# Performance work log

Hardware: AMD Instinct MI355X
Metric: run time of the kernel (lower is better)

## Reference

```python
import jax, jax.numpy as jnp
import numpy as np

B, S, D = 4, 2048, 1024
H, DH = 16, 64
THETA = 10000.0


def _rope_tables(seq_len, dim):
    # freqs_cis = exp(i * t * f), here as cos/sin tables, shape [S, dim//2]
    freqs = 1.0 / (THETA ** (jnp.arange(0, dim, 2, dtype=jnp.float32) / dim))
    ang = jnp.outer(jnp.arange(seq_len, dtype=jnp.float32), freqs)
    return jnp.cos(ang), jnp.sin(ang)


def _apply_rope(x, cos, sin):
    # x: [B,S,H,DH]; pairs are interleaved (x[...,2i], x[...,2i+1])
    xe = x[..., 0::2]
    xo = x[..., 1::2]
    c = cos[None, :, None, :]
    s = sin[None, :, None, :]
    out = jnp.stack([xe * c - xo * s, xe * s + xo * c], axis=-1)
    return out.reshape(x.shape).astype(x.dtype)


def setup_inputs() -> dict:
    key = jax.random.key(0)
    ks = jax.random.split(key, 5)
    x = jax.random.normal(ks[0], (B, S, D), dtype=jnp.float32)
    Wq = jax.random.normal(ks[1], (D, D), dtype=jnp.float32) * 0.02
    Wk = jax.random.normal(ks[2], (D, D), dtype=jnp.float32) * 0.02
    Wv = jax.random.normal(ks[3], (D, D), dtype=jnp.float32) * 0.02
    Wo = jax.random.normal(ks[4], (D, D), dtype=jnp.float32) * 0.02
    lambdas = jnp.zeros((2,), dtype=jnp.float32)
    return {"x": x, "Wq": Wq, "Wk": Wk, "Wv": Wv, "Wo": Wo, "lambdas": lambdas}


def reference(x, Wq, Wk, Wv, Wo, lambdas):
    scale = 1.0 / np.sqrt(DH)
    q = (x @ Wq.T).reshape(B, S, H, DH)
    k = (x @ Wk.T).reshape(B, S, H, DH)
    v = (x @ Wv.T).reshape(B, S, H, DH)
    cos, sin = _rope_tables(S, DH)
    q = _apply_rope(q, cos, sin)
    k = _apply_rope(k, cos, sin)
    # explicit QK^T with causal mask, softmax, then @V (dropout is identity in eval)
    attn = jnp.einsum('bshd,bthd->bhst', q, k) * scale  # [B,H,S,S]
    causal = jnp.tril(jnp.ones((S, S), dtype=bool))
    attn = jnp.where(causal[None, None], attn, -jnp.inf)
    probs = jax.nn.softmax(attn, axis=-1)
    head_out = jnp.einsum('bhst,bthd->bshd', probs, v)  # [B,S,H,DH]
    out = head_out.reshape(B, S, D) @ Wo.T
    return out
```

## Files before the change

kernel.cpp:

```cpp
#include <hip/hip_runtime.h>
#include <math.h>

static constexpr int Bsz = 4, Sq = 2048, Dm = 1024, NH = 16, DHd = 64;
static constexpr int Mrows = Bsz * Sq;
static constexpr float ROPE_LN = 0.14391156831212787f;
static constexpr float QSCALE = 0.18033688011112043f;

typedef _Float16 half8 __attribute__((ext_vector_type(8)));
typedef _Float16 half4v __attribute__((ext_vector_type(4)));
typedef __fp16 fp16x2 __attribute__((ext_vector_type(2)));
typedef float f32x4 __attribute__((ext_vector_type(4)));

__device__ __forceinline__ void gl_lds16(const void* g, void* l) {
    __builtin_amdgcn_global_load_lds(
        (const __attribute__((address_space(1))) void*)g,
        (__attribute__((address_space(3))) void*)l, 16, 0, 0);
}

__device__ __forceinline__ float exp2_hw(float x) {
    float r;
    asm volatile("v_exp_f32 %0, %1" : "=v"(r) : "v"(x));
    return r;
}

__global__ __launch_bounds__(256) void prep_kernel(
    const float* __restrict__ x,
    const float* __restrict__ Wq, const float* __restrict__ Wk,
    const float* __restrict__ Wv, const float* __restrict__ Wo,
    _Float16* __restrict__ xh,
    _Float16* __restrict__ Wqh, _Float16* __restrict__ Wkh,
    _Float16* __restrict__ Wvh, _Float16* __restrict__ Woh,
    float2* __restrict__ rope)
{
    const int i = blockIdx.x * 256 + threadIdx.x;
    if (i < 2097152) {
        const float4 v = ((const float4*)x)[i];
        half4v hv;
        hv[0] = (_Float16)v.x; hv[1] = (_Float16)v.y;
        hv[2] = (_Float16)v.z; hv[3] = (_Float16)v.w;
        ((half4v*)xh)[i] = hv;
    } else if (i < 3145728) {
        const int w = (i - 2097152) >> 18;
        const int off = (i - 2097152) & 262143;
        const float* s = (w == 0) ? Wq : (w == 1) ? Wk : (w == 2) ? Wv : Wo;
        _Float16* d = (w == 0) ? Wqh : (w == 1) ? Wkh : (w == 2) ? Wvh : Woh;
        const float sc = (w == 0) ? QSCALE : 1.0f;
        const float4 v = ((const float4*)s)[off];
        half4v hv;
        hv[0] = (_Float16)(v.x * sc); hv[1] = (_Float16)(v.y * sc);
        hv[2] = (_Float16)(v.z * sc); hv[3] = (_Float16)(v.w * sc);
        ((half4v*)d)[off] = hv;
    } else {
        const int t = i - 3145728;
        const int pos = t >> 5, j = t & 31;
        const float f = expf(-ROPE_LN * (float)(2 * j));
        const float a = (float)pos * f;
        rope[t] = make_float2(cosf(a), sinf(a));
    }
}

template <typename OutT, int MODE>
__device__ __forceinline__ void mfma_gemm_body(
    _Float16 (*As)[128 * 32], _Float16 (*Bs)[128 * 32],
    const _Float16* __restrict__ A, const _Float16* __restrict__ W,
    OutT* __restrict__ C, const float2* __restrict__ rope, int K, int N,
    int m0, int n0)
{
    const int tid = threadIdx.x;
    const int wave = tid >> 6, lane = tid & 63;
    const int quad = lane >> 4, l16 = lane & 15;
    const int wm = (wave >> 2) * 64;
    const int wn = (wave & 3) * 32;

    const int rr = tid >> 2, cp = tid & 3;
    const int cc = cp ^ ((rr >> 1) & 3);
    const _Float16* gA = A + (size_t)(m0 + rr) * K + cc * 8;
    const _Float16* gB = W + (size_t)(n0 + rr) * K + cc * 8;
    const int lOff = wave * 512;

    const int sw = (l16 >> 1) & 3;
    int offA[4], offB[2];
    #pragma unroll
    for (int t = 0; t < 4; ++t)
        offA[t] = (wm + t * 16 + l16) * 32 + ((quad ^ sw) * 8);
    #pragma unroll
    for (int t = 0; t < 2; ++t)
        offB[t] = (wn + t * 16 + l16) * 32 + ((quad ^ sw) * 8);

    f32x4 acc[4][2];
    #pragma unroll
    for (int im = 0; im < 4; ++im)
        #pragma unroll
        for (int nb = 0; nb < 2; ++nb)
            #pragma unroll
            for (int r = 0; r < 4; ++r) acc[im][nb][r] = 0.f;

    for (int k0 = 0; k0 < K; k0 += 64) {
        __syncthreads();
        #pragma unroll
        for (int kh = 0; kh < 2; ++kh) {
            gl_lds16(gA + k0 + kh * 32, &As[kh][lOff]);
            gl_lds16(gB + k0 + kh * 32, &Bs[kh][lOff]);
        }
        __syncthreads();

        #pragma unroll
        for (int kh = 0; kh < 2; ++kh) {
            half8 a[4], b[2];
            #pragma unroll
            for (int t = 0; t < 4; ++t)
                a[t] = *(const half8*)&As[kh][offA[t]];
            #pragma unroll
            for (int t = 0; t < 2; ++t)
                b[t] = *(const half8*)&Bs[kh][offB[t]];
            #pragma unroll
            for (int im = 0; im < 4; ++im)
                #pragma unroll
                for (int nb = 0; nb < 2; ++nb)
                    acc[im][nb] = __builtin_amdgcn_mfma_f32_16x16x32_f16(
                        a[im], b[nb], acc[im][nb], 0, 0, 0);
        }
    }

    #pragma unroll
    for (int nb = 0; nb < 2; ++nb) {
        const int n = n0 + wn + nb * 16 + l16;
        if constexpr (MODE == 2) {
            const int hb = ((m0 + wm) >> 11) * 16 + (n >> 6);
            const int dh = n & 63;
            const int tb = (m0 + wm) & (Sq - 1);
            half8 v0, v1;
            #pragma unroll
            for (int r = 0; r < 4; ++r)
                #pragma unroll
                for (int im = 0; im < 4; ++im) {
                    const int idx = r * 4 + im;
                    const _Float16 h = (_Float16)acc[im][nb][r];
                    if (idx < 8) v0[idx] = h; else v1[idx - 8] = h;
                }
            _Float16* dst = C + (((size_t)hb * 64 + dh) << 11) + tb + quad * 16;
            *(half8*)dst = v0;
            *(half8*)(dst + 8) = v1;
        } else {
            const int j = (n & 63) >> 1;
            #pragma unroll
            for (int im = 0; im < 4; ++im) {
                #pragma unroll
                for (int r = 0; r < 4; ++r) {
                    const int m = m0 + wm + im * 16 + quad * 4 + r;
                    float v = acc[im][nb][r];
                    if constexpr (MODE == 1) {
                        const int pos = m & (Sq - 1);
                        const float2 cs = rope[pos * 32 + j];
                        const float vp = __shfl_xor(v, 1);
                        v = (n & 1) ? (vp * cs.y + v * cs.x)
                                    : (v * cs.x - vp * cs.y);
                        C[(size_t)m * N + n] = (_Float16)v;
                    } else {
                        C[(size_t)m * N + n] = v;
                    }
                }
            }
        }
    }
}

__device__ __forceinline__ void xcd_swizzle(int& m0, int& n0) {
    const int orig = blockIdx.x + (blockIdx.y << 3);
    const int xcd = orig & 7, j = orig >> 3;
    m0 = (xcd * 8 + (j >> 3)) * 128;
    n0 = (j & 7) * 128;
}

__global__ __launch_bounds__(512) void qkv_mfma_kernel(
    const _Float16* __restrict__ xh,
    const _Float16* __restrict__ Wq, const _Float16* __restrict__ Wk,
    const _Float16* __restrict__ Wv,
    _Float16* __restrict__ Qo, _Float16* __restrict__ Ko,
    _Float16* __restrict__ VTp, const float2* __restrict__ rope)
{
    __shared__ _Float16 As[2][128 * 32];
    __shared__ _Float16 Bs[2][128 * 32];
    int m0, n0;
    xcd_swizzle(m0, n0);
    const int z = blockIdx.z;
    if (z == 0)
        mfma_gemm_body<_Float16, 1>(As, Bs, xh, Wq, Qo, rope, Dm, Dm, m0, n0);
    else if (z == 1)
        mfma_gemm_body<_Float16, 1>(As, Bs, xh, Wk, Ko, rope, Dm, Dm, m0, n0);
    else
        mfma_gemm_body<_Float16, 2>(As, Bs, xh, Wv, VTp, nullptr, Dm, Dm,
                                    m0, n0);
}

__global__ __launch_bounds__(512) void oproj_mfma_kernel(
    const _Float16* __restrict__ HOh, const _Float16* __restrict__ Wo,
    float* __restrict__ out)
{
    __shared__ _Float16 As[2][128 * 32];
    __shared__ _Float16 Bs[2][128 * 32];
    int m0, n0;
    xcd_swizzle(m0, n0);
    mfma_gemm_body<float, 0>(As, Bs, HOh, Wo, out, nullptr, Dm, Dm, m0, n0);
}

__global__ __launch_bounds__(256) void attn_mfma_kernel(
    const _Float16* __restrict__ Q, const _Float16* __restrict__ K,
    const _Float16* __restrict__ VT, _Float16* __restrict__ HO)
{
    __shared__ _Float16 Ks[2][64 * 64];
    __shared__ _Float16 Vs[2][64 * 64];
    __shared__ _Float16 Ps[4][32][72];

    const int tid = threadIdx.x;
    const int wave = tid >> 6, lane = tid & 63;
    const int quad = lane >> 4, l16 = lane & 15;
    const int id = blockIdx.x;
    const int hb = id & 63;
    const int qi = 15 - (id >> 6);
    const int h = hb & 15, b = hb >> 4;
    const int q0 = qi * 128;
    const size_t base = (size_t)b * Sq * Dm + (size_t)h * DHd;
    const size_t vtbase = (size_t)hb * 64 * Sq;

    half8 ones;
    #pragma unroll
    for (int i = 0; i < 8; ++i) ones[i] = (_Float16)1.0f;

    half8 aQ[2][2];
    #pragma unroll
    for (int mf = 0; mf < 2; ++mf) {
        const _Float16* qrow =
            Q + base + (size_t)(q0 + wave * 32 + mf * 16 + l16) * Dm + quad * 8;
        aQ[mf][0] = *(const half8*)(qrow);
        aQ[mf][1] = *(const half8*)(qrow + 32);
    }

    f32x4 Oacc[2][4];
    #pragma unroll
    for (int mf = 0; mf < 2; ++mf)
        #pragma unroll
        for (int nb = 0; nb < 4; ++nb)
            #pragma unroll
            for (int r = 0; r < 4; ++r) Oacc[mf][nb][r] = 0.f;
    f32x4 lacc[2];
    #pragma unroll
    for (int mf = 0; mf < 2; ++mf)
        #pragma unroll
        for (int r = 0; r < 4; ++r) lacc[mf][r] = 0.f;

    auto stage_tile = [&](int t0, int buf) {
        #pragma unroll
        for (int i = 0; i < 2; ++i) {
            const int F = (wave * 2 + i) * 64 + lane;
            const int r = F >> 3;
            const int cl = (F & 7) ^ (r & 7);
            gl_lds16(K + base + (size_t)(t0 + r) * Dm + cl * 8,
                     &Ks[buf][(wave * 2 + i) * 512]);
            gl_lds16(VT + vtbase + ((size_t)r << 11) + t0 + cl * 8,
                     &Vs[buf][(wave * 2 + i) * 512]);
        }
    };

    auto do_tile = [&](int buf, int dd, bool diag) {
        const _Float16* Kb = Ks[buf];
        const _Float16* Vb = Vs[buf];

        f32x4 sacc[2][4];
        #pragma unroll
        for (int mf = 0; mf < 2; ++mf)
            #pragma unroll
            for (int nb = 0; nb < 4; ++nb)
                #pragma unroll
                for (int r = 0; r < 4; ++r) sacc[mf][nb][r] = 0.f;
        __builtin_amdgcn_s_setprio(1);
        #pragma unroll
        for (int kstep = 0; kstep < 2; ++kstep) {
            #pragma unroll
            for (int nb = 0; nb < 4; ++nb) {
                const int krow = nb * 16 + l16;
                const int kch = (kstep * 4 + quad) ^ (krow & 7);
                const half8 bK = *(const half8*)&Kb[krow * 64 + kch * 8];
                #pragma unroll
                for (int mf = 0; mf < 2; ++mf)
                    sacc[mf][nb] = __builtin_amdgcn_mfma_f32_16x16x32_f16(
                        aQ[mf][kstep], bK, sacc[mf][nb], 0, 0, 0);
            }
        }
        __builtin_amdgcn_s_setprio(0);

        #pragma unroll
        for (int mf = 0; mf < 2; ++mf)
            #pragma unroll
            for (int r = 0; r < 4; ++r) {
                float e[4];
                #pragma unroll
                for (int nb = 0; nb < 4; ++nb) {
                    float v = sacc[mf][nb][r];
                    if (diag && (nb * 16 + l16 + dd >
                                 wave * 32 + mf * 16 + quad * 4 + r))
                        v = -1.0e4f;
                    e[nb] = exp2_hw(v);
                }
                const fp16x2 lo = __builtin_amdgcn_cvt_pkrtz(e[0], e[1]);
                const fp16x2 hi = __builtin_amdgcn_cvt_pkrtz(e[2], e[3]);
                uint2 pk;
                pk.x = __builtin_bit_cast(unsigned int, lo);
                pk.y = __builtin_bit_cast(unsigned int, hi);
                *(uint2*)&Ps[wave][mf * 16 + quad * 4 + r][l16 * 4] = pk;
            }

        __builtin_amdgcn_s_setprio(1);
        #pragma unroll
        for (int kstep = 0; kstep < 2; ++kstep) {
            half8 aP[2];
            #pragma unroll
            for (int mf = 0; mf < 2; ++mf) {
                aP[mf] = *(const half8*)
                    &Ps[wave][mf * 16 + l16][kstep * 32 + quad * 8];
                lacc[mf] = __builtin_amdgcn_mfma_f32_16x16x32_f16(
                    aP[mf], ones, lacc[mf], 0, 0, 0);
            }
            #pragma unroll
            for (int nb = 0; nb < 4; ++nb) {
                const int vrow = nb * 16 + l16;
                const int vch = (kstep * 4 + quad) ^ (vrow & 7);
                const half8 bV = *(const half8*)&Vb[vrow * 64 + vch * 8];
                #pragma unroll
                for (int mf = 0; mf < 2; ++mf)
                    Oacc[mf][nb] = __builtin_amdgcn_mfma_f32_16x16x32_f16(
                        aP[mf], bV, Oacc[mf][nb], 0, 0, 0);
            }
        }
        __builtin_amdgcn_s_setprio(0);
    };

    const int nt = 2 * qi + 2;
    stage_tile(0, 0);
    for (int t = 0; t < nt; ++t) {
        __syncthreads();
        if (t + 1 < nt) stage_tile((t + 1) * 64, (t + 1) & 1);
        do_tile(t & 1, t * 64 - q0, t >= nt - 2);
    }

    #pragma unroll
    for (int mf = 0; mf < 2; ++mf) {
        float inv[4];
        #pragma unroll
        for (int r = 0; r < 4; ++r) inv[r] = 1.0f / lacc[mf][r];
        #pragma unroll
        for (int nb = 0; nb < 4; ++nb)
            #pragma unroll
            for (int r = 0; r < 4; ++r) {
                const int row = wave * 32 + mf * 16 + quad * 4 + r;
                HO[base + (size_t)(q0 + row) * Dm + nb * 16 + l16] =
                    (_Float16)(Oacc[mf][nb][r] * inv[r]);
            }
    }
}

extern "C" void kernel_launch(void* const* d_in, const int* in_sizes, int n_in,
                              void* d_out, int out_size, void* d_ws, size_t ws_size,
                              hipStream_t stream)
{
    const float* x  = (const float*)d_in[0];
    const float* Wq = (const float*)d_in[1];
    const float* Wk = (const float*)d_in[2];
    const float* Wv = (const float*)d_in[3];
    const float* Wo = (const float*)d_in[4];
    float* out = (float*)d_out;

    const size_t matX = (size_t)Mrows * Dm;
    const size_t matW = (size_t)Dm * Dm;

    _Float16* xh  = (_Float16*)d_ws;
    _Float16* Wqh = xh + matX;
    _Float16* Wkh = Wqh + matW;
    _Float16* Wvh = Wkh + matW;
    _Float16* Woh = Wvh + matW;
    _Float16* Qh  = Woh + matW;
    _Float16* Kh  = Qh + matX;
    _Float16* VTp = Kh + matX;
    _Float16* HOh = VTp + matX;
    float2* rope  = (float2*)(HOh + matX);

    dim3 blk(256);
    prep_kernel<<<(3145728 + 65536) / 256, blk, 0, stream>>>(
        x, Wq, Wk, Wv, Wo, xh, Wqh, Wkh, Wvh, Woh, rope);
    qkv_mfma_kernel<<<dim3(Dm / 128, Mrows / 128, 3), dim3(512), 0, stream>>>(
        xh, Wqh, Wkh, Wvh, Qh, Kh, VTp, rope);
    attn_mfma_kernel<<<dim3(16 * NH * Bsz), blk, 0, stream>>>(
        Qh, Kh, VTp, HOh);
    oproj_mfma_kernel<<<dim3(Dm / 128, Mrows / 128, 1), dim3(512), 0, stream>>>(
        HOh, Woh, out);
}
```

Before: 236.7 us.

## Triple-buffer GEMM LDS tiles with async prefetch two k-steps ahead

Replaces the synchronous load-then-compute loop in the shared MFMA GEMM body with a three-slot ring buffer. Global-to-LDS loads are issued two 32-wide k-steps ahead and waited on with vmcnt counters, so memory latency overlaps with MFMA work. The QKV and output-projection kernels grow their LDS tiles from 2 to 3 slots. This costs more LDS per block, which may reduce occupancy, and it relies on vmcnt counting matching exactly the two loads issued per stage.

```diff
diff --git a/kernel.cpp b/kernel.cpp
--- a/kernel.cpp
+++ b/kernel.cpp
@@ -95,31 +95,43 @@
             #pragma unroll
             for (int r = 0; r < 4; ++r) acc[im][nb][r] = 0.f;
 
-    for (int k0 = 0; k0 < K; k0 += 64) {
-        __syncthreads();
-        #pragma unroll
-        for (int kh = 0; kh < 2; ++kh) {
-            gl_lds16(gA + k0 + kh * 32, &As[kh][lOff]);
-            gl_lds16(gB + k0 + kh * 32, &Bs[kh][lOff]);
-        }
-        __syncthreads();
-
-        #pragma unroll
-        for (int kh = 0; kh < 2; ++kh) {
-            half8 a[4], b[2];
-            #pragma unroll
-            for (int t = 0; t < 4; ++t)
-                a[t] = *(const half8*)&As[kh][offA[t]];
-            #pragma unroll
-            for (int t = 0; t < 2; ++t)
-                b[t] = *(const half8*)&Bs[kh][offB[t]];
-            #pragma unroll
-            for (int im = 0; im < 4; ++im)
-                #pragma unroll
-                for (int nb = 0; nb < 2; ++nb)
-                    acc[im][nb] = __builtin_amdgcn_mfma_f32_16x16x32_f16(
-                        a[im], b[nb], acc[im][nb], 0, 0, 0);
-        }
+    auto stage = [&](int s, int t) {
+        const int koff = t * 32;
+        gl_lds16(gA + koff, &As[s][lOff]);
+        gl_lds16(gB + koff, &Bs[s][lOff]);
+    };
+
+    const int KS = K >> 5;
+    stage(0, 0);
+    stage(1, 1);
+    int slot = 0, ps = 2;
+    for (int t = 0; t < KS; ++t) {
+        if (t < KS - 1)
+            asm volatile("s_waitcnt vmcnt(2)" ::: "memory");
+        else
+            asm volatile("s_waitcnt vmcnt(0)" ::: "memory");
+        __builtin_amdgcn_s_barrier();
+
+        if (t + 2 < KS) stage(ps, t + 2);
+
+        const _Float16* Ab = As[slot];
+        const _Float16* Bb = Bs[slot];
+        half8 a[4], b[2];
+        #pragma unroll
+        for (int q = 0; q < 4; ++q)
+            a[q] = *(const half8*)&Ab[offA[q]];
+        #pragma unroll
+        for (int q = 0; q < 2; ++q)
+            b[q] = *(const half8*)&Bb[offB[q]];
+        #pragma unroll
+        for (int im = 0; im < 4; ++im)
+            #pragma unroll
+            for (int nb = 0; nb < 2; ++nb)
+                acc[im][nb] = __builtin_amdgcn_mfma_f32_16x16x32_f16(
+                    a[im], b[nb], acc[im][nb], 0, 0, 0);
+
+        slot = (slot == 2) ? 0 : slot + 1;
+        ps = (ps == 2) ? 0 : ps + 1;
     }
 
     #pragma unroll
@@ -179,8 +191,8 @@
     _Float16* __restrict__ Qo, _Float16* __restrict__ Ko,
     _Float16* __restrict__ VTp, const float2* __restrict__ rope)
 {
-    __shared__ _Float16 As[2][128 * 32];
-    __shared__ _Float16 Bs[2][128 * 32];
+    __shared__ _Float16 As[3][128 * 32];
+    __shared__ _Float16 Bs[3][128 * 32];
     int m0, n0;
     xcd_swizzle(m0, n0);
     const int z = blockIdx.z;
@@ -197,8 +209,8 @@
     const _Float16* __restrict__ HOh, const _Float16* __restrict__ Wo,
     float* __restrict__ out)
 {
-    __shared__ _Float16 As[2][128 * 32];
-    __shared__ _Float16 Bs[2][128 * 32];
+    __shared__ _Float16 As[3][128 * 32];
+    __shared__ _Float16 Bs[3][128 * 32];
     int m0, n0;
     xcd_swizzle(m0, n0);
     mfma_gemm_body<float, 0>(As, Bs, HOh, Wo, out, nullptr, Dm, Dm, m0, n0);
```

New measurement: 254.1 us. 1.07x slower.
